# Optimization experiments

Measured on AMD Instinct MI355X. Metric: run time of the kernel, lower is better.

The kernel has to match this reference:

```python
import jax, jax.numpy as jnp
import numpy as np

B, C, H, W = 16, 512, 48, 48


def setup_inputs() -> dict:
    key = jax.random.key(0)
    k1, k2 = jax.random.split(key)
    rgb = jax.random.normal(k1, (B, C, H, W), dtype=jnp.float32)
    depth = jax.random.normal(k2, (B, C, H, W), dtype=jnp.float32)
    return {"rgb": rgb, "depth": depth}


def reference(rgb, depth):
    b, c, h, w = rgb.shape
    hw = h * w
    q = rgb.reshape(b, c, hw)              # [B, C, HW]
    k = depth.reshape(b, c, hw)            # [B, C, HW]
    # channel-affinity: energy[b, i, j] = <rgb_chan_i, depth_chan_j>
    energy = jnp.einsum('bcn,bdn->bcd', q, k)   # [B, C, C]
    cl_index = jnp.argmax(energy, axis=2)       # [B, C] best-matching depth channel per rgb channel
    # gather matched depth channels and fuse
    gathered = depth[jnp.arange(b)[:, None], cl_index]  # [B, C, H, W]
    return rgb + gathered
```

## Files before the change

kernel.cpp:

```cpp
#include <hip/hip_runtime.h>
#include <stdint.h>

#define BATCH 16
#define CH    512
#define HW    2304
#define BM    128
#define BN    128
#define BK    32
#define NKT   (HW / BK)

typedef _Float16 half8  __attribute__((ext_vector_type(8)));
typedef float    f32x16 __attribute__((ext_vector_type(16)));

#define AH_OFF 0
#define AL_OFF 8192
#define BH_OFF 16384
#define BL_OFF 24576
#define BUF_SZ 32768

#define MFMA16 __builtin_amdgcn_mfma_f32_32x32x16_f16

__device__ __forceinline__ uint32_t f32_sortable(float f) {
    uint32_t u = __float_as_uint(f);
    return (u & 0x80000000u) ? ~u : (u | 0x80000000u);
}

__device__ __forceinline__ int swz(int r, int cb) {
    return r * 64 + (cb ^ (((r >> 1) & 3) << 4));
}

__device__ __forceinline__ void cvt8(const float4& v0, const float4& v1,
                                     half8& h, half8& l) {
    float vv[8] = {v0.x, v0.y, v0.z, v0.w, v1.x, v1.y, v1.z, v1.w};
    #pragma unroll
    for (int j = 0; j < 8; ++j) {
        _Float16 hh = (_Float16)vv[j];
        h[j] = hh;
        l[j] = (_Float16)(vv[j] - (float)hh);
    }
}

__device__ __forceinline__ void load_tile(const float* aG, const float* bG, int k0,
                                          float4 (&av)[2], float4 (&bv)[2], int q) {
    av[0] = *(const float4*)(aG + k0 + q * 8 + 0);
    av[1] = *(const float4*)(aG + k0 + q * 8 + 4);
    bv[0] = *(const float4*)(bG + k0 + q * 8 + 0);
    bv[1] = *(const float4*)(bG + k0 + q * 8 + 4);
}

__device__ __forceinline__ void stage_tile(char* dst,
                                           const float4 (&av)[2], const float4 (&bv)[2],
                                           int row, int q) {
    half8 h, l;
    cvt8(av[0], av[1], h, l);
    *(half8*)(dst + AH_OFF + swz(row, q * 16)) = h;
    *(half8*)(dst + AL_OFF + swz(row, q * 16)) = l;
    cvt8(bv[0], bv[1], h, l);
    *(half8*)(dst + BH_OFF + swz(row, q * 16)) = h;
    *(half8*)(dst + BL_OFF + swz(row, q * 16)) = l;
}

__device__ __forceinline__ void compute_tile(const char* buf, int rA0, int rB, int hb,
                                             f32x16& acc0, f32x16& acc1) {
    #pragma unroll
    for (int kc = 0; kc < 2; ++kc) {
        const int cb = kc * 32 + hb;
        half8 ah0 = *(const half8*)(buf + AH_OFF + swz(rA0,      cb));
        half8 ah1 = *(const half8*)(buf + AH_OFF + swz(rA0 + 32, cb));
        half8 al0 = *(const half8*)(buf + AL_OFF + swz(rA0,      cb));
        half8 al1 = *(const half8*)(buf + AL_OFF + swz(rA0 + 32, cb));
        half8 bh  = *(const half8*)(buf + BH_OFF + swz(rB, cb));
        half8 bl  = *(const half8*)(buf + BL_OFF + swz(rB, cb));
        acc0 = MFMA16(ah0, bh, acc0, 0, 0, 0);
        acc1 = MFMA16(ah1, bh, acc1, 0, 0, 0);
        acc0 = MFMA16(ah0, bl, acc0, 0, 0, 0);
        acc1 = MFMA16(ah1, bl, acc1, 0, 0, 0);
        acc0 = MFMA16(al0, bh, acc0, 0, 0, 0);
        acc1 = MFMA16(al1, bh, acc1, 0, 0, 0);
    }
}

__global__ __launch_bounds__(512, 1)
void energy_argmax_kernel(const float* __restrict__ q,
                          const float* __restrict__ kmat,
                          unsigned long long* __restrict__ best)
{
    const int bid = blockIdx.x;
    const int nid = (bid & 7) * 32 + (bid >> 3);
    const int d0  = (nid & 3) * BN;
    const int c0  = ((nid >> 2) & 3) * BM;
    const int b   = nid >> 4;

    const int tid = threadIdx.x;
    const int lane = tid & 63;
    const int w    = tid >> 6;
    const int wm   = w >> 2;
    const int wn   = w & 3;

    __shared__ __align__(16) char sm[2 * BUF_SZ];
    char* buf0 = sm;
    char* buf1 = sm + BUF_SZ;

    const float* qb = q    + (size_t)b * CH * HW;
    const float* kb = kmat + (size_t)b * CH * HW;

    const int row = tid >> 2, sq = tid & 3;
    const float* aG = qb + (size_t)(c0 + row) * HW;
    const float* bG = kb + (size_t)(d0 + row) * HW;

    float4 av0[2], bv0[2], av1[2], bv1[2];

    load_tile(aG, bG, 0, av0, bv0, sq);
    stage_tile(buf0, av0, bv0, row, sq);
    load_tile(aG, bG, BK, av1, bv1, sq);
    __syncthreads();

    f32x16 acc0 = {}, acc1 = {};

    const int rA0 = wm * 64 + (lane & 31);
    const int rB  = wn * 32 + (lane & 31);
    const int hb  = (lane >> 5) * 16;

    for (int kt = 0; kt < NKT; kt += 2) {
        if (kt + 2 < NKT) load_tile(aG, bG, (kt + 2) * BK, av0, bv0, sq);
        compute_tile(buf0, rA0, rB, hb, acc0, acc1);
        stage_tile(buf1, av1, bv1, row, sq);
        __syncthreads();
        if (kt + 3 < NKT) load_tile(aG, bG, (kt + 3) * BK, av1, bv1, sq);
        compute_tile(buf1, rA0, rB, hb, acc0, acc1);
        if (kt + 2 < NKT) stage_tile(buf0, av0, bv0, row, sq);
        __syncthreads();
    }

    const uint32_t didx = ~(uint32_t)(d0 + wn * 32 + (lane & 31));
    #pragma unroll
    for (int mi = 0; mi < 2; ++mi) {
        #pragma unroll
        for (int qr = 0; qr < 16; ++qr) {
            float v = (mi == 0) ? acc0[qr] : acc1[qr];
            int rowl = wm * 64 + mi * 32 + (qr & 3) + 8 * (qr >> 2) + 4 * (lane >> 5);
            unsigned long long p =
                ((unsigned long long)f32_sortable(v) << 32) | didx;
            #pragma unroll
            for (int off = 1; off < 32; off <<= 1) {
                unsigned long long o = __shfl_xor(p, off, 64);
                if (o > p) p = o;
            }
            if ((lane & 31) == 0)
                atomicMax(&best[(size_t)b * CH + c0 + rowl], p);
        }
    }
}

__global__ __launch_bounds__(256)
void gather_add_kernel(const float* __restrict__ rgb,
                       const float* __restrict__ depth,
                       const unsigned long long* __restrict__ best,
                       float* __restrict__ out)
{
    const int row = blockIdx.x;
    const int b   = row >> 9;
    const uint32_t idx = ~(uint32_t)(best[row] & 0xFFFFFFFFull);
    const float4* src = (const float4*)(rgb   + (size_t)row * HW);
    const float4* dep = (const float4*)(depth + ((size_t)b * CH + idx) * HW);
    float4*       dst = (float4*)(out + (size_t)row * HW);
    for (int j = threadIdx.x; j < HW / 4; j += 256) {
        float4 a = src[j], d = dep[j];
        float4 r; r.x = a.x + d.x; r.y = a.y + d.y; r.z = a.z + d.z; r.w = a.w + d.w;
        dst[j] = r;
    }
}

extern "C" void kernel_launch(void* const* d_in, const int* in_sizes, int n_in,
                              void* d_out, int out_size, void* d_ws, size_t ws_size,
                              hipStream_t stream)
{
    const float* rgb   = (const float*)d_in[0];
    const float* depth = (const float*)d_in[1];
    float* out = (float*)d_out;
    unsigned long long* best = (unsigned long long*)d_ws;

    hipMemsetAsync(best, 0, (size_t)BATCH * CH * sizeof(unsigned long long), stream);

    energy_argmax_kernel<<<256, 512, 0, stream>>>(rgb, depth, best);

    gather_add_kernel<<<BATCH * CH, 256, 0, stream>>>(rgb, depth, best, out);
}
```

Before: 119.3 us.

## Halve GEMM M-tile to 64 rows, use 256-thread blocks with two blocks per CU

Shrinks the energy GEMM tile from 128x128 to 64x128, launching 512 blocks of 256 threads (4 waves) with launch bounds allowing two blocks per CU. The load and stage mapping changes so each thread stages one A chunk and two B chunks. Barriers become an explicit lgkmcnt wait plus s_barrier, and MFMA sections run at raised wave priority. The aim is better CU coverage on the 256-CU part and overlap between co-resident blocks, paid for with more global re-reads of B per unit of work and more atomics.

```diff
diff --git a/kernel.cpp b/kernel.cpp
--- a/kernel.cpp
+++ b/kernel.cpp
@@ -4,7 +4,7 @@
 #define BATCH 16
 #define CH    512
 #define HW    2304
-#define BM    128
+#define BM    64
 #define BN    128
 #define BK    32
 #define NKT   (HW / BK)
@@ -13,12 +13,18 @@
 typedef float    f32x16 __attribute__((ext_vector_type(16)));
 
 #define AH_OFF 0
-#define AL_OFF 8192
-#define BH_OFF 16384
-#define BL_OFF 24576
-#define BUF_SZ 32768
+#define AL_OFF 4096
+#define BH_OFF 8192
+#define BL_OFF 16384
+#define BUF_SZ 24576
 
 #define MFMA16 __builtin_amdgcn_mfma_f32_32x32x16_f16
+
+#define LGKM_BARRIER() do { \
+    asm volatile("s_waitcnt lgkmcnt(0)" ::: "memory"); \
+    __builtin_amdgcn_s_barrier(); \
+    __builtin_amdgcn_sched_barrier(0); \
+} while (0)
 
 __device__ __forceinline__ uint32_t f32_sortable(float f) {
     uint32_t u = __float_as_uint(f);
@@ -41,27 +47,33 @@
 }
 
 __device__ __forceinline__ void load_tile(const float* aG, const float* bG, int k0,
-                                          float4 (&av)[2], float4 (&bv)[2], int q) {
-    av[0] = *(const float4*)(aG + k0 + q * 8 + 0);
-    av[1] = *(const float4*)(aG + k0 + q * 8 + 4);
-    bv[0] = *(const float4*)(bG + k0 + q * 8 + 0);
-    bv[1] = *(const float4*)(bG + k0 + q * 8 + 4);
+                                          float4 (&av)[2], float4 (&bv)[4]) {
+    av[0] = *(const float4*)(aG + k0 + 0);
+    av[1] = *(const float4*)(aG + k0 + 4);
+    bv[0] = *(const float4*)(bG + k0 + 0);
+    bv[1] = *(const float4*)(bG + k0 + 4);
+    bv[2] = *(const float4*)(bG + k0 + 8);
+    bv[3] = *(const float4*)(bG + k0 + 12);
 }
 
 __device__ __forceinline__ void stage_tile(char* dst,
-                                           const float4 (&av)[2], const float4 (&bv)[2],
-                                           int row, int q) {
-    half8 h, l;
-    cvt8(av[0], av[1], h, l);
-    *(half8*)(dst + AH_OFF + swz(row, q * 16)) = h;
-    *(half8*)(dst + AL_OFF + swz(row, q * 16)) = l;
-    cvt8(bv[0], bv[1], h, l);
-    *(half8*)(dst + BH_OFF + swz(row, q * 16)) = h;
-    *(half8*)(dst + BL_OFF + swz(row, q * 16)) = l;
+                                           const float4 (&av)[2], const float4 (&bv)[4],
+                                           int arow, int q, int brow, int h) {
+    half8 hh, ll;
+    cvt8(av[0], av[1], hh, ll);
+    *(half8*)(dst + AH_OFF + swz(arow, q * 16)) = hh;
+    *(half8*)(dst + AL_OFF + swz(arow, q * 16)) = ll;
+    cvt8(bv[0], bv[1], hh, ll);
+    *(half8*)(dst + BH_OFF + swz(brow, h * 32)) = hh;
+    *(half8*)(dst + BL_OFF + swz(brow, h * 32)) = ll;
+    cvt8(bv[2], bv[3], hh, ll);
+    *(half8*)(dst + BH_OFF + swz(brow, h * 32 + 16)) = hh;
+    *(half8*)(dst + BL_OFF + swz(brow, h * 32 + 16)) = ll;
 }
 
 __device__ __forceinline__ void compute_tile(const char* buf, int rA0, int rB, int hb,
                                              f32x16& acc0, f32x16& acc1) {
+    __builtin_amdgcn_s_setprio(1);
     #pragma unroll
     for (int kc = 0; kc < 2; ++kc) {
         const int cb = kc * 32 + hb;
@@ -78,24 +90,23 @@
         acc0 = MFMA16(al0, bh, acc0, 0, 0, 0);
         acc1 = MFMA16(al1, bh, acc1, 0, 0, 0);
     }
-}
-
-__global__ __launch_bounds__(512, 1)
+    __builtin_amdgcn_s_setprio(0);
+}
+
+__global__ __launch_bounds__(256, 2)
 void energy_argmax_kernel(const float* __restrict__ q,
                           const float* __restrict__ kmat,
                           unsigned long long* __restrict__ best)
 {
     const int bid = blockIdx.x;
-    const int nid = (bid & 7) * 32 + (bid >> 3);
+    const int nid = (bid & 7) * 64 + (bid >> 3);
     const int d0  = (nid & 3) * BN;
-    const int c0  = ((nid >> 2) & 3) * BM;
-    const int b   = nid >> 4;
-
-    const int tid = threadIdx.x;
+    const int c0  = ((nid >> 2) & 7) * BM;
+    const int b   = nid >> 5;
+
+    const int tid  = threadIdx.x;
     const int lane = tid & 63;
     const int w    = tid >> 6;
-    const int wm   = w >> 2;
-    const int wn   = w & 3;
 
     __shared__ __align__(16) char sm[2 * BUF_SZ];
     char* buf0 = sm;
@@ -104,41 +115,42 @@
     const float* qb = q    + (size_t)b * CH * HW;
     const float* kb = kmat + (size_t)b * CH * HW;
 
-    const int row = tid >> 2, sq = tid & 3;
-    const float* aG = qb + (size_t)(c0 + row) * HW;
-    const float* bG = kb + (size_t)(d0 + row) * HW;
-
-    float4 av0[2], bv0[2], av1[2], bv1[2];
-
-    load_tile(aG, bG, 0, av0, bv0, sq);
-    stage_tile(buf0, av0, bv0, row, sq);
-    load_tile(aG, bG, BK, av1, bv1, sq);
-    __syncthreads();
+    const int arow = tid >> 2, aq = tid & 3;
+    const int brow = tid >> 1, bh = tid & 1;
+    const float* aG = qb + (size_t)(c0 + arow) * HW + aq * 8;
+    const float* bG = kb + (size_t)(d0 + brow) * HW + bh * 16;
+
+    float4 av0[2], bv0[4], av1[2], bv1[4];
+
+    load_tile(aG, bG, 0, av0, bv0);
+    stage_tile(buf0, av0, bv0, arow, aq, brow, bh);
+    load_tile(aG, bG, BK, av1, bv1);
+    LGKM_BARRIER();
 
     f32x16 acc0 = {}, acc1 = {};
 
-    const int rA0 = wm * 64 + (lane & 31);
-    const int rB  = wn * 32 + (lane & 31);
+    const int rA0 = lane & 31;
+    const int rB  = w * 32 + (lane & 31);
     const int hb  = (lane >> 5) * 16;
 
     for (int kt = 0; kt < NKT; kt += 2) {
-        if (kt + 2 < NKT) load_tile(aG, bG, (kt + 2) * BK, av0, bv0, sq);
+        if (kt + 2 < NKT) load_tile(aG, bG, (kt + 2) * BK, av0, bv0);
         compute_tile(buf0, rA0, rB, hb, acc0, acc1);
-        stage_tile(buf1, av1, bv1, row, sq);
-        __syncthreads();
-        if (kt + 3 < NKT) load_tile(aG, bG, (kt + 3) * BK, av1, bv1, sq);
+        stage_tile(buf1, av1, bv1, arow, aq, brow, bh);
+        LGKM_BARRIER();
+        if (kt + 3 < NKT) load_tile(aG, bG, (kt + 3) * BK, av1, bv1);
         compute_tile(buf1, rA0, rB, hb, acc0, acc1);
-        if (kt + 2 < NKT) stage_tile(buf0, av0, bv0, row, sq);
-        __syncthreads();
-    }
-
-    const uint32_t didx = ~(uint32_t)(d0 + wn * 32 + (lane & 31));
+        if (kt + 2 < NKT) stage_tile(buf0, av0, bv0, arow, aq, brow, bh);
+        LGKM_BARRIER();
+    }
+
+    const uint32_t didx = ~(uint32_t)(d0 + w * 32 + (lane & 31));
     #pragma unroll
     for (int mi = 0; mi < 2; ++mi) {
         #pragma unroll
         for (int qr = 0; qr < 16; ++qr) {
             float v = (mi == 0) ? acc0[qr] : acc1[qr];
-            int rowl = wm * 64 + mi * 32 + (qr & 3) + 8 * (qr >> 2) + 4 * (lane >> 5);
+            int rowl = mi * 32 + (qr & 3) + 8 * (qr >> 2) + 4 * (lane >> 5);
             unsigned long long p =
                 ((unsigned long long)f32_sortable(v) << 32) | didx;
             #pragma unroll
@@ -182,7 +194,7 @@
 
     hipMemsetAsync(best, 0, (size_t)BATCH * CH * sizeof(unsigned long long), stream);
 
-    energy_argmax_kernel<<<256, 512, 0, stream>>>(rgb, depth, best);
+    energy_argmax_kernel<<<512, 256, 0, stream>>>(rgb, depth, best);
 
     gather_add_kernel<<<BATCH * CH, 256, 0, stream>>>(rgb, depth, best, out);
 }
```

Result: slower. 130.0 us (+9.0%).

## Double K tile depth and reorder LDS staging ahead of MFMA compute

Applied to the files above, without the earlier changes.

Raises the K tile from 32 to 64, so each thread loads 16 floats per row and double-buffered LDS grows to 128 KB with a wider 8-slot XOR swizzle. The loop now stages the next buffer before computing on the current one. It uses a custom barrier (lgkmcnt wait, s_barrier, sched_barrier) and raises wave priority around the MFMA block. The intent is to halve the number of barriers and loop iterations and to overlap LDS writes with MFMA work. The cost is more registers for the prefetch values and LDS use near the per-CU limit.

```diff
diff --git a/kernel.cpp b/kernel.cpp
--- a/kernel.cpp
+++ b/kernel.cpp
@@ -6,27 +6,33 @@
 #define HW    2304
 #define BM    128
 #define BN    128
-#define BK    32
+#define BK    64
 #define NKT   (HW / BK)
 
 typedef _Float16 half8  __attribute__((ext_vector_type(8)));
 typedef float    f32x16 __attribute__((ext_vector_type(16)));
 
 #define AH_OFF 0
-#define AL_OFF 8192
-#define BH_OFF 16384
-#define BL_OFF 24576
-#define BUF_SZ 32768
+#define AL_OFF 16384
+#define BH_OFF 32768
+#define BL_OFF 49152
+#define BUF_SZ 65536
 
 #define MFMA16 __builtin_amdgcn_mfma_f32_32x32x16_f16
+
+#define LGKM_BARRIER() do { \
+    asm volatile("s_waitcnt lgkmcnt(0)" ::: "memory"); \
+    __builtin_amdgcn_s_barrier(); \
+    __builtin_amdgcn_sched_barrier(0); \
+} while (0)
 
 __device__ __forceinline__ uint32_t f32_sortable(float f) {
     uint32_t u = __float_as_uint(f);
     return (u & 0x80000000u) ? ~u : (u | 0x80000000u);
 }
 
-__device__ __forceinline__ int swz(int r, int cb) {
-    return r * 64 + (cb ^ (((r >> 1) & 3) << 4));
+__device__ __forceinline__ int swz(int r, int s) {
+    return r * 128 + ((s ^ ((r >> 1) & 7)) << 4);
 }
 
 __device__ __forceinline__ void cvt8(const float4& v0, const float4& v1,
@@ -41,36 +47,47 @@
 }
 
 __device__ __forceinline__ void load_tile(const float* aG, const float* bG, int k0,
-                                          float4 (&av)[2], float4 (&bv)[2], int q) {
-    av[0] = *(const float4*)(aG + k0 + q * 8 + 0);
-    av[1] = *(const float4*)(aG + k0 + q * 8 + 4);
-    bv[0] = *(const float4*)(bG + k0 + q * 8 + 0);
-    bv[1] = *(const float4*)(bG + k0 + q * 8 + 4);
+                                          float4 (&av)[4], float4 (&bv)[4]) {
+    av[0] = *(const float4*)(aG + k0 + 0);
+    av[1] = *(const float4*)(aG + k0 + 4);
+    av[2] = *(const float4*)(aG + k0 + 8);
+    av[3] = *(const float4*)(aG + k0 + 12);
+    bv[0] = *(const float4*)(bG + k0 + 0);
+    bv[1] = *(const float4*)(bG + k0 + 4);
+    bv[2] = *(const float4*)(bG + k0 + 8);
+    bv[3] = *(const float4*)(bG + k0 + 12);
 }
 
 __device__ __forceinline__ void stage_tile(char* dst,
-                                           const float4 (&av)[2], const float4 (&bv)[2],
+                                           const float4 (&av)[4], const float4 (&bv)[4],
                                            int row, int q) {
     half8 h, l;
     cvt8(av[0], av[1], h, l);
-    *(half8*)(dst + AH_OFF + swz(row, q * 16)) = h;
-    *(half8*)(dst + AL_OFF + swz(row, q * 16)) = l;
+    *(half8*)(dst + AH_OFF + swz(row, 2 * q))     = h;
+    *(half8*)(dst + AL_OFF + swz(row, 2 * q))     = l;
+    cvt8(av[2], av[3], h, l);
+    *(half8*)(dst + AH_OFF + swz(row, 2 * q + 1)) = h;
+    *(half8*)(dst + AL_OFF + swz(row, 2 * q + 1)) = l;
     cvt8(bv[0], bv[1], h, l);
-    *(half8*)(dst + BH_OFF + swz(row, q * 16)) = h;
-    *(half8*)(dst + BL_OFF + swz(row, q * 16)) = l;
-}
-
-__device__ __forceinline__ void compute_tile(const char* buf, int rA0, int rB, int hb,
+    *(half8*)(dst + BH_OFF + swz(row, 2 * q))     = h;
+    *(half8*)(dst + BL_OFF + swz(row, 2 * q))     = l;
+    cvt8(bv[2], bv[3], h, l);
+    *(half8*)(dst + BH_OFF + swz(row, 2 * q + 1)) = h;
+    *(half8*)(dst + BL_OFF + swz(row, 2 * q + 1)) = l;
+}
+
+__device__ __forceinline__ void compute_tile(const char* buf, int rA0, int rB, int half,
                                              f32x16& acc0, f32x16& acc1) {
+    __builtin_amdgcn_s_setprio(1);
     #pragma unroll
-    for (int kc = 0; kc < 2; ++kc) {
-        const int cb = kc * 32 + hb;
-        half8 ah0 = *(const half8*)(buf + AH_OFF + swz(rA0,      cb));
-        half8 ah1 = *(const half8*)(buf + AH_OFF + swz(rA0 + 32, cb));
-        half8 al0 = *(const half8*)(buf + AL_OFF + swz(rA0,      cb));
-        half8 al1 = *(const half8*)(buf + AL_OFF + swz(rA0 + 32, cb));
-        half8 bh  = *(const half8*)(buf + BH_OFF + swz(rB, cb));
-        half8 bl  = *(const half8*)(buf + BL_OFF + swz(rB, cb));
+    for (int kc = 0; kc < 4; ++kc) {
+        const int s0 = 2 * kc + half;
+        half8 ah0 = *(const half8*)(buf + AH_OFF + swz(rA0,      s0));
+        half8 ah1 = *(const half8*)(buf + AH_OFF + swz(rA0 + 32, s0));
+        half8 al0 = *(const half8*)(buf + AL_OFF + swz(rA0,      s0));
+        half8 al1 = *(const half8*)(buf + AL_OFF + swz(rA0 + 32, s0));
+        half8 bh  = *(const half8*)(buf + BH_OFF + swz(rB, s0));
+        half8 bl  = *(const half8*)(buf + BL_OFF + swz(rB, s0));
         acc0 = MFMA16(ah0, bh, acc0, 0, 0, 0);
         acc1 = MFMA16(ah1, bh, acc1, 0, 0, 0);
         acc0 = MFMA16(ah0, bl, acc0, 0, 0, 0);
@@ -78,6 +95,7 @@
         acc0 = MFMA16(al0, bh, acc0, 0, 0, 0);
         acc1 = MFMA16(al1, bh, acc1, 0, 0, 0);
     }
+    __builtin_amdgcn_s_setprio(0);
 }
 
 __global__ __launch_bounds__(512, 1)
@@ -91,7 +109,7 @@
     const int c0  = ((nid >> 2) & 3) * BM;
     const int b   = nid >> 4;
 
-    const int tid = threadIdx.x;
+    const int tid  = threadIdx.x;
     const int lane = tid & 63;
     const int w    = tid >> 6;
     const int wm   = w >> 2;
@@ -105,31 +123,31 @@
     const float* kb = kmat + (size_t)b * CH * HW;
 
     const int row = tid >> 2, sq = tid & 3;
-    const float* aG = qb + (size_t)(c0 + row) * HW;
-    const float* bG = kb + (size_t)(d0 + row) * HW;
-
-    float4 av0[2], bv0[2], av1[2], bv1[2];
-
-    load_tile(aG, bG, 0, av0, bv0, sq);
+    const float* aG = qb + (size_t)(c0 + row) * HW + sq * 16;
+    const float* bG = kb + (size_t)(d0 + row) * HW + sq * 16;
+
+    float4 av0[4], bv0[4], av1[4], bv1[4];
+
+    load_tile(aG, bG, 0, av0, bv0);
     stage_tile(buf0, av0, bv0, row, sq);
-    load_tile(aG, bG, BK, av1, bv1, sq);
-    __syncthreads();
+    load_tile(aG, bG, BK, av1, bv1);
+    LGKM_BARRIER();
 
     f32x16 acc0 = {}, acc1 = {};
 
-    const int rA0 = wm * 64 + (lane & 31);
-    const int rB  = wn * 32 + (lane & 31);
-    const int hb  = (lane >> 5) * 16;
-
-    for (int kt = 0; kt < NKT; kt += 2) {
-        if (kt + 2 < NKT) load_tile(aG, bG, (kt + 2) * BK, av0, bv0, sq);
-        compute_tile(buf0, rA0, rB, hb, acc0, acc1);
+    const int rA0  = wm * 64 + (lane & 31);
+    const int rB   = wn * 32 + (lane & 31);
+    const int half = lane >> 5;
+
+    for (int kt = 0; kt < NKT - 1; kt += 2) {
+        if (kt + 2 < NKT) load_tile(aG, bG, (kt + 2) * BK, av0, bv0);
         stage_tile(buf1, av1, bv1, row, sq);
-        __syncthreads();
-        if (kt + 3 < NKT) load_tile(aG, bG, (kt + 3) * BK, av1, bv1, sq);
-        compute_tile(buf1, rA0, rB, hb, acc0, acc1);
+        compute_tile(buf0, rA0, rB, half, acc0, acc1);
+        LGKM_BARRIER();
+        if (kt + 3 < NKT) load_tile(aG, bG, (kt + 3) * BK, av1, bv1);
         if (kt + 2 < NKT) stage_tile(buf0, av0, bv0, row, sq);
-        __syncthreads();
+        compute_tile(buf1, rA0, rB, half, acc0, acc1);
+        LGKM_BARRIER();
     }
 
     const uint32_t didx = ~(uint32_t)(d0 + wn * 32 + (lane & 31));
```

New measurement: 123.2 us. +3.3%, slower.
